# Kernel tuning notes

Hardware: AMD Instinct MI355X
Metric: run time of the kernel (lower is better)

The kernel has to match this reference:

```python
import jax, jax.numpy as jnp
import numpy as np
from jax import lax

B, T = 256, 64
X_DIMS, CCG_DIMS, H, N_TAG = 512, 256, 1024, 512
DIN = X_DIMS + CCG_DIMS
PAD = 0


def setup_inputs() -> dict:
    key = jax.random.key(0)
    ks = jax.random.split(key, 12)
    emb = jax.random.normal(ks[0], (N_TAG, CCG_DIMS), jnp.float32)
    emb = emb.at[PAD].set(0.0)  # padding_idx row is zero
    s_ih = 1.0 / np.sqrt(H)
    return {
        "x": jax.random.normal(ks[1], (B, X_DIMS), jnp.float32),
        "atom_truth": jax.random.randint(ks[2], (B, T), 0, N_TAG),
        "atom_mask": jax.random.randint(ks[3], (B, T), 0, 2).astype(bool),
        "emb": emb,
        "W_ih": jax.random.normal(ks[4], (4 * H, DIN), jnp.float32) * s_ih,
        "W_hh": jax.random.normal(ks[5], (4 * H, H), jnp.float32) * s_ih,
        "b_ih": jax.random.normal(ks[6], (4 * H,), jnp.float32) * s_ih,
        "b_hh": jax.random.normal(ks[7], (4 * H,), jnp.float32) * s_ih,
        "W_out": jax.random.normal(ks[8], (N_TAG, H), jnp.float32) * s_ih,
        "b_out": jax.random.normal(ks[9], (N_TAG,), jnp.float32) * s_ih,
        "h0": jax.random.normal(ks[10], (B, H), jnp.float32),
        "c0": jax.random.normal(ks[11], (B, H), jnp.float32),
    }


def reference(x, atom_truth, atom_mask, emb, W_ih, W_hh, b_ih, b_hh, W_out, b_out, h0, c0):
    b, t = atom_truth.shape
    # teacher forcing: step 0 uses token 0, step k uses atom_truth[:, k-1]
    prev_tok = jnp.concatenate([jnp.zeros((b, 1), atom_truth.dtype), atom_truth[:, :-1]], axis=1)
    ccg = emb[prev_tok]                                      # [B,T,E]
    inp = jnp.concatenate([jnp.broadcast_to(x[:, None, :], (b, t, x.shape[1])), ccg], axis=-1)
    # precompute input projection for all steps: [B,T,4H]
    xproj = jnp.einsum('btd,gd->btg', inp, W_ih) + b_ih + b_hh

    def cell(carry, xt):                                     # xt: [B,4H]
        h, c = carry
        gates = xt + h @ W_hh.T
        i, f, g, o = jnp.split(gates, 4, axis=-1)            # torch gate order i,f,g,o
        i, f, o = jax.nn.sigmoid(i), jax.nn.sigmoid(f), jax.nn.sigmoid(o)
        g = jnp.tanh(g)
        c = f * c + i * g
        h = o * jnp.tanh(c)
        return (h, c), h

    _, hs = lax.scan(cell, (h0, c0), jnp.swapaxes(xproj, 0, 1))  # hs: [T,B,H]
    logits = hs @ W_out.T + b_out                            # [T,B,N_TAG]
    logp = jax.nn.log_softmax(logits, axis=-1)
    tgt = atom_truth.T                                       # [T,B]
    nll = -jnp.take_along_axis(logp, tgt[..., None], axis=-1)[..., 0]  # [T,B]
    mask = atom_mask.T.astype(nll.dtype)
    return jnp.sum(nll * mask) / jnp.sum(mask)


if __name__ == "__main__":
    print(reference(**setup_inputs()))
```

## Files before the change

kernel.cpp:

```cpp
#include <hip/hip_runtime.h>
#include <hip/hip_bf16.h>

#define BB 256
#define TT 64
#define XD 512
#define CCG 256
#define DINk 768
#define HH 1024
#define G4 4096
#define NTAG 512

typedef float f32x4 __attribute__((ext_vector_type(4)));
typedef short s16x8 __attribute__((ext_vector_type(8)));
typedef short s16x4 __attribute__((ext_vector_type(4)));

#define WS_HS    0ull
#define WS_XBASE (WS_HS + (size_t)(TT+1)*BB*HH*2)
#define WS_EPROJ (WS_XBASE + (size_t)BB*G4*4)
#define WS_WIH   (WS_EPROJ + (size_t)NTAG*G4*4)
#define WS_WOUT  (WS_WIH + (size_t)G4*DINk*2)
#define WS_XBF   (WS_WOUT + (size_t)NTAG*HH*2)
#define WS_EMBBF (WS_XBF + (size_t)BB*XD*2)
#define WS_CNT   (WS_EMBBF + (size_t)NTAG*CCG*2)
#define WS_ACC   (WS_CNT + 1024)
#define WS_FLAG  (WS_ACC + 64)
#define WS_XPROJ (WS_FLAG + 64)

static __device__ __forceinline__ short f2bf(float f) {
  __hip_bfloat16 h = __float2bfloat16(f);
  return __builtin_bit_cast(short, h);
}
static __device__ __forceinline__ float bf2f(unsigned short u) {
  unsigned x = ((unsigned)u) << 16;
  return __builtin_bit_cast(float, x);
}
static __device__ __forceinline__ void store_dword_cc(void* p, unsigned v) {
  asm volatile("global_store_dword %0, %1, off sc0 sc1" :: "v"(p), "v"(v) : "memory");
}
static __device__ __forceinline__ void store_short_cc(void* p, unsigned v) {
  asm volatile("global_store_short %0, %1, off sc0 sc1" :: "v"(p), "v"(v) : "memory");
}
static __device__ __forceinline__ int load_int_cc(const void* p) {
  int r;
  asm volatile("global_load_dword %0, %1, off sc0 sc1\n\ts_waitcnt vmcnt(0)"
               : "=v"(r) : "v"(p) : "memory");
  return r;
}
static __device__ __forceinline__ float fsig(float x) {
  return __builtin_amdgcn_rcpf(1.f + __expf(-x));
}
static __device__ __forceinline__ float ftanh(float x) {
  return 1.f - 2.f * __builtin_amdgcn_rcpf(1.f + __expf(2.f * x));
}

__global__ void k_f2bf8(const float* __restrict__ in, short* __restrict__ out, int n8) {
  int i = blockIdx.x * blockDim.x + threadIdx.x;
  if (i >= n8) return;
  size_t idx = (size_t)i * 8;
  float4 a = *(const float4*)(in + idx);
  float4 b = *(const float4*)(in + idx + 4);
  s16x8 o;
  o[0]=f2bf(a.x); o[1]=f2bf(a.y); o[2]=f2bf(a.z); o[3]=f2bf(a.w);
  o[4]=f2bf(b.x); o[5]=f2bf(b.y); o[6]=f2bf(b.z); o[7]=f2bf(b.w);
  *(s16x8*)(out + idx) = o;
}

__global__ void k_init(const float* __restrict__ h0, const int* __restrict__ mask_as_int,
                       char* __restrict__ ws) {
  int tid = blockIdx.x * blockDim.x + threadIdx.x;
  short* hb0 = (short*)(ws + WS_HS);
  for (int i = tid; i < BB * HH; i += gridDim.x * blockDim.x) hb0[i] = f2bf(h0[i]);
  if (blockIdx.x == 0) {
    int* cnt = (int*)(ws + WS_CNT);
    for (int i = threadIdx.x; i < 256; i += blockDim.x) cnt[i] = 0;
    int v = 0;
    for (int i = threadIdx.x; i < 4096; i += blockDim.x) v |= (mask_as_int[i] & ~1);
    __shared__ int red[256];
    red[threadIdx.x] = v;
    __syncthreads();
    if (threadIdx.x == 0) {
      int a = 0;
      for (int j = 0; j < 256; j++) a |= red[j];
      ((int*)(ws + WS_FLAG))[0] = (a != 0) ? 1 : 0;
      float* acc = (float*)(ws + WS_ACC);
      acc[0] = 0.f; acc[1] = 0.f;
    }
  }
}

__global__ __launch_bounds__(256) void k_gemm(const short* __restrict__ A, int lda,
    const short* __restrict__ Bm, int ldb, int bcol0,
    short* __restrict__ C, int ldc, int ksteps,
    const float* __restrict__ bias1, const float* __restrict__ bias2) {
  int w = threadIdx.x >> 6, l = threadIdx.x & 63;
  int lc = l & 15, lq = l >> 4;
  int arow = blockIdx.x * 64 + w * 16 + lc;
  f32x4 acc[4];
  const f32x4 z = {0.f, 0.f, 0.f, 0.f};
#pragma unroll
  for (int i = 0; i < 4; i++) acc[i] = z;
  const short* ap = A + (size_t)arow * lda + lq * 8;
  for (int kk = 0; kk < ksteps; ++kk) {
    s16x8 a = *(const s16x8*)(ap + kk * 32);
#pragma unroll
    for (int nt = 0; nt < 4; ++nt) {
      int brow = blockIdx.y * 64 + nt * 16 + lc;
      s16x8 b = *(const s16x8*)(Bm + (size_t)brow * ldb + bcol0 + kk * 32 + lq * 8);
      acc[nt] = __builtin_amdgcn_mfma_f32_16x16x32_bf16(a, b, acc[nt], 0, 0, 0);
    }
  }
#pragma unroll
  for (int nt = 0; nt < 4; ++nt) {
    int col = blockIdx.y * 64 + nt * 16 + lc;
    float badd = (bias1 ? bias1[col] : 0.f) + (bias2 ? bias2[col] : 0.f);
#pragma unroll
    for (int j = 0; j < 4; j++) {
      int r = blockIdx.x * 64 + w * 16 + lq * 4 + j;
      C[(size_t)r * ldc + col] = f2bf(acc[nt][j] + badd);
    }
  }
}

__global__ __launch_bounds__(256) void k_xproj_t(const short* __restrict__ xb,
    const short* __restrict__ ep, const int* __restrict__ atruth,
    short* __restrict__ out) {
  __shared__ short tile[64 * 264];
  const int cc = blockIdx.x, g = blockIdx.y, t = blockIdx.z;
  const int b = threadIdx.x;
  const int tok = (t == 0) ? 0 : atruth[b * TT + t - 1];
  const int gc0 = g * 1024 + cc * 64;
  const short* xs = xb + (size_t)b * G4 + gc0;
  const short* es = ep + (size_t)tok * G4 + gc0;
#pragma unroll
  for (int i = 0; i < 64; i += 8) {
    s16x8 xv = *(const s16x8*)(xs + i);
    s16x8 ev = *(const s16x8*)(es + i);
#pragma unroll
    for (int j = 0; j < 8; ++j)
      tile[(i + j) * 264 + b] = f2bf(bf2f((unsigned short)xv[j]) + bf2f((unsigned short)ev[j]));
  }
  __syncthreads();
  const int c = threadIdx.x >> 2, b0 = (threadIdx.x & 3) * 64;
  short* dst = out + ((size_t)t * G4 + gc0 + c) * BB + b0;
  const short* src = tile + c * 264 + b0;
#pragma unroll
  for (int i = 0; i < 64; i += 8) *(s16x8*)(dst + i) = *(const s16x8*)(src + i);
}

__global__ __launch_bounds__(512, 2) void k_lstm(const float* __restrict__ Whh,
    const short* __restrict__ xproj, const float* __restrict__ c0,
    char* __restrict__ ws) {
  extern __shared__ char sm[];
  float* part = (float*)(sm + 131072);
  const int bid = blockIdx.x;
  const int xcd = bid & 7, slot = bid >> 3;
  const int mg = xcd >> 1;
  const int hb = slot * 2 + (xcd & 1);
  const int wgid = (xcd & 1) * 32 + slot;
  const int tid = threadIdx.x;
  const int w = tid >> 6, l = tid & 63;
  const int lc = l & 15, lq = l >> 4;
  const int wy = w & 3, kh = w >> 2;

  {
    const int r = tid >> 3, q = tid & 7;
    const int g = r >> 4, rl = r & 15;
    const float* src = Whh + (size_t)(g * HH + hb * 16 + rl) * HH + q * 128;
    const int swz = (rl & 7) << 4;
    char* dst = sm + r * 2048;
#pragma unroll
    for (int i = 0; i < 128; i += 8) {
      float4 f0 = *(const float4*)(src + i);
      float4 f1 = *(const float4*)(src + i + 4);
      s16x8 o;
      o[0]=f2bf(f0.x); o[1]=f2bf(f0.y); o[2]=f2bf(f0.z); o[3]=f2bf(f0.w);
      o[4]=f2bf(f1.x); o[5]=f2bf(f1.y); o[6]=f2bf(f1.z); o[7]=f2bf(f1.w);
      int koff = (q * 128 + i) * 2;
      *(s16x8*)(dst + (koff ^ swz)) = o;
    }
  }

  const int colbase = hb * 16;
  short* hs = (short*)(ws + WS_HS);
  int* flags = (int*)(ws + WS_CNT);
  const int swzl = (lc & 7) << 4;
  const int row0 = mg * 64 + wy * 16;

  float cst[4];
  s16x4 xg0, xg1, xg2, xg3, xn0, xn1, xn2, xn3;
  if (kh == 0) {
#pragma unroll
    for (int j = 0; j < 4; ++j)
      cst[j] = c0[(size_t)(row0 + lq * 4 + j) * HH + colbase + lc];
    const short* xp = xproj + ((size_t)colbase + lc) * BB + row0 + lq * 4;
    xg0 = *(const s16x4*)(xp);
    xg1 = *(const s16x4*)(xp + (size_t)1024 * BB);
    xg2 = *(const s16x4*)(xp + (size_t)2048 * BB);
    xg3 = *(const s16x4*)(xp + (size_t)3072 * BB);
  }
  float* pslot = part + (size_t)wy * 1024 + l;
  __syncthreads();

  for (int t = 0; t < TT; ++t) {
    if (t && w == 0) {
      const int* f = flags + mg * 64 + l;
      for (;;) {
        int v = load_int_cc(f);
        if (__all(v >= t)) break;
        __builtin_amdgcn_s_sleep(1);
      }
    }
    __syncthreads();

    if (kh == 0 && t + 1 < TT) {
      const short* xp = xproj + ((size_t)(t + 1) * G4 + colbase + lc) * BB + row0 + lq * 4;
      xn0 = *(const s16x4*)(xp);
      xn1 = *(const s16x4*)(xp + (size_t)1024 * BB);
      xn2 = *(const s16x4*)(xp + (size_t)2048 * BB);
      xn3 = *(const s16x4*)(xp + (size_t)3072 * BB);
    }

    const short* arowp = hs + (size_t)t * (BB * HH) + (size_t)(row0 + lc) * HH + kh * 512 + lq * 8;
    s16x8 areg[16];
#pragma unroll
    for (int kk = 0; kk < 16; ++kk) areg[kk] = *(const s16x8*)(arowp + kk * 32);

    const f32x4 z = {0.f, 0.f, 0.f, 0.f};
    f32x4 acc0 = z, acc1 = z, acc2 = z, acc3 = z;
#pragma unroll
    for (int kk = 0; kk < 16; ++kk) {
      const int kx = (((kh * 16 + kk) * 64) + lq * 16) ^ swzl;
      const char* bp = sm + lc * 2048 + kx;
      acc0 = __builtin_amdgcn_mfma_f32_16x16x32_bf16(areg[kk], *(const s16x8*)(bp), acc0, 0, 0, 0);
      acc1 = __builtin_amdgcn_mfma_f32_16x16x32_bf16(areg[kk], *(const s16x8*)(bp + 16 * 2048), acc1, 0, 0, 0);
      acc2 = __builtin_amdgcn_mfma_f32_16x16x32_bf16(areg[kk], *(const s16x8*)(bp + 32 * 2048), acc2, 0, 0, 0);
      acc3 = __builtin_amdgcn_mfma_f32_16x16x32_bf16(areg[kk], *(const s16x8*)(bp + 48 * 2048), acc3, 0, 0, 0);
    }

    if (kh == 1) {
#pragma unroll
      for (int j = 0; j < 4; ++j) {
        pslot[(0 * 4 + j) * 64] = acc0[j];
        pslot[(1 * 4 + j) * 64] = acc1[j];
        pslot[(2 * 4 + j) * 64] = acc2[j];
        pslot[(3 * 4 + j) * 64] = acc3[j];
      }
    }
    __syncthreads();

    if (kh == 0) {
#pragma unroll
      for (int j = 0; j < 4; ++j) {
        acc0[j] += pslot[(0 * 4 + j) * 64];
        acc1[j] += pslot[(1 * 4 + j) * 64];
        acc2[j] += pslot[(2 * 4 + j) * 64];
        acc3[j] += pslot[(3 * 4 + j) * 64];
      }
      short* hrow = hs + (size_t)(t + 1) * (BB * HH) +
                    (size_t)(row0 + lq * 4) * HH + colbase + lc;
#pragma unroll
      for (int j = 0; j < 4; ++j) {
        float pi = acc0[j] + bf2f((unsigned short)xg0[j]);
        float pf = acc1[j] + bf2f((unsigned short)xg1[j]);
        float pg = acc2[j] + bf2f((unsigned short)xg2[j]);
        float po = acc3[j] + bf2f((unsigned short)xg3[j]);
        float cv = fsig(pf) * cst[j] + fsig(pi) * ftanh(pg);
        cst[j] = cv;
        store_short_cc(hrow + (size_t)j * HH, (unsigned)(unsigned short)f2bf(fsig(po) * ftanh(cv)));
      }
      xg0 = xn0; xg1 = xn1; xg2 = xn2; xg3 = xn3;
    }
    asm volatile("s_waitcnt vmcnt(0)" ::: "memory");
    __syncthreads();
    if (tid == 0 && t < TT - 1) store_dword_cc(flags + mg * 64 + wgid, t + 1);
  }
}

__global__ __launch_bounds__(256, 1) void k_logits(const short* __restrict__ hsb,
    const short* __restrict__ Wo, const float* __restrict__ bout,
    const int* __restrict__ atruth, const void* __restrict__ maskp,
    char* __restrict__ ws) {
  extern __shared__ char sm[];
  const int tid = threadIdx.x;
  const int w = tid >> 6, l = tid & 63;
  const int lc = l & 15, lq = l >> 4;
  const int rowbase = blockIdx.x * 64 + w * 16;
  f32x4 acc[32];
#pragma unroll
  for (int nt = 0; nt < 32; ++nt) {
    float bv = bout[nt * 16 + lc];
    f32x4 tmp = {bv, bv, bv, bv};
    acc[nt] = tmp;
  }
  const int swzl = (lc & 7) << 4;
  for (int kb = 0; kb < 16; ++kb) {
    __syncthreads();
    {
      const int r0 = tid >> 3, q = tid & 7;
#pragma unroll
      for (int i = 0; i < 16; i++) {
        int r = r0 + 32 * i;
        s16x8 v = *(const s16x8*)(Wo + (size_t)r * HH + kb * 64 + q * 8);
        *(s16x8*)(sm + r * 128 + ((q * 16) ^ ((r & 7) << 4))) = v;
      }
    }
    __syncthreads();
#pragma unroll
    for (int ks = 0; ks < 2; ++ks) {
      s16x8 a = *(const s16x8*)(hsb + (size_t)(rowbase + lc) * HH + kb * 64 + ks * 32 + lq * 8);
      const int kx = (ks * 64 + lq * 16) ^ swzl;
#pragma unroll
      for (int nt = 0; nt < 32; ++nt) {
        s16x8 b = *(const s16x8*)(sm + (nt * 16 + lc) * 128 + kx);
        acc[nt] = __builtin_amdgcn_mfma_f32_16x16x32_bf16(a, b, acc[nt], 0, 0, 0);
      }
    }
  }
  const int bytemode = ((const int*)(ws + WS_FLAG))[0];
  const unsigned char* mb = (const unsigned char*)maskp;
  const int* mi = (const int*)maskp;
  float nlls = 0.f, cnts = 0.f;
#pragma unroll
  for (int j = 0; j < 4; j++) {
    int gr = rowbase + lq * 4 + j;
    int tt = gr >> 8, b = gr & 255;
    float m = -1e30f;
#pragma unroll
    for (int nt = 0; nt < 32; ++nt) m = fmaxf(m, acc[nt][j]);
    m = fmaxf(m, __shfl_xor(m, 1)); m = fmaxf(m, __shfl_xor(m, 2));
    m = fmaxf(m, __shfl_xor(m, 4)); m = fmaxf(m, __shfl_xor(m, 8));
    float s = 0.f;
#pragma unroll
    for (int nt = 0; nt < 32; ++nt) s += __expf(acc[nt][j] - m);
    s += __shfl_xor(s, 1); s += __shfl_xor(s, 2);
    s += __shfl_xor(s, 4); s += __shfl_xor(s, 8);
    float lse = m + __logf(s);
    int tg = atruth[b * TT + tt];
    int mk = bytemode ? (int)mb[b * TT + tt] : mi[b * TT + tt];
    if (((tg & 15) == lc) && mk) {
      float tl = 0.f;
#pragma unroll
      for (int nt = 0; nt < 32; ++nt) if (nt == (tg >> 4)) tl = acc[nt][j];
      nlls += (lse - tl);
    }
    if (lc == 0 && mk) cnts += 1.f;
  }
#pragma unroll
  for (int off = 1; off < 64; off <<= 1) {
    nlls += __shfl_xor(nlls, off);
    cnts += __shfl_xor(cnts, off);
  }
  if (l == 0) {
    float* accf = (float*)(ws + WS_ACC);
    atomicAdd(&accf[0], nlls);
    atomicAdd(&accf[1], cnts);
  }
}

__global__ void k_final(const char* __restrict__ ws, float* __restrict__ out) {
  const float* accf = (const float*)(ws + WS_ACC);
  out[0] = accf[0] / accf[1];
}

extern "C" void kernel_launch(void* const* d_in, const int* in_sizes, int n_in,
                              void* d_out, int out_size, void* d_ws, size_t ws_size,
                              hipStream_t stream) {
  const float* x      = (const float*)d_in[0];
  const int*   atruth = (const int*)d_in[1];
  const void*  amask  = d_in[2];
  const float* emb    = (const float*)d_in[3];
  const float* W_ih   = (const float*)d_in[4];
  const float* W_hh   = (const float*)d_in[5];
  const float* b_ih   = (const float*)d_in[6];
  const float* b_hh   = (const float*)d_in[7];
  const float* W_out  = (const float*)d_in[8];
  const float* b_out  = (const float*)d_in[9];
  const float* h0     = (const float*)d_in[10];
  const float* c0     = (const float*)d_in[11];
  char* ws = (char*)d_ws;
  float* out = (float*)d_out;

  hipFuncSetAttribute((const void*)k_lstm, hipFuncAttributeMaxDynamicSharedMemorySize, 147456);
  hipFuncSetAttribute((const void*)k_logits, hipFuncAttributeMaxDynamicSharedMemorySize, 65536);

  k_f2bf8<<<dim3((G4 * DINk / 8 + 255) / 256), 256, 0, stream>>>(W_ih, (short*)(ws + WS_WIH), G4 * DINk / 8);
  k_f2bf8<<<dim3((NTAG * HH / 8 + 255) / 256), 256, 0, stream>>>(W_out, (short*)(ws + WS_WOUT), NTAG * HH / 8);
  k_f2bf8<<<dim3((BB * XD / 8 + 255) / 256), 256, 0, stream>>>(x, (short*)(ws + WS_XBF), BB * XD / 8);
  k_f2bf8<<<dim3((NTAG * CCG / 8 + 255) / 256), 256, 0, stream>>>(emb, (short*)(ws + WS_EMBBF), NTAG * CCG / 8);

  k_init<<<64, 256, 0, stream>>>(h0, (const int*)amask, ws);

  k_gemm<<<dim3(4, 64), 256, 0, stream>>>((short*)(ws + WS_XBF), XD, (short*)(ws + WS_WIH), DINk, 0,
                                          (short*)(ws + WS_XBASE), G4, XD / 32, b_ih, b_hh);
  k_gemm<<<dim3(8, 64), 256, 0, stream>>>((short*)(ws + WS_EMBBF), CCG, (short*)(ws + WS_WIH), DINk, XD,
                                          (short*)(ws + WS_EPROJ), G4, CCG / 32, nullptr, nullptr);

  k_xproj_t<<<dim3(16, 4, 64), 256, 0, stream>>>((const short*)(ws + WS_XBASE),
                                                 (const short*)(ws + WS_EPROJ), atruth,
                                                 (short*)(ws + WS_XPROJ));

  k_lstm<<<256, 512, 147456, stream>>>(W_hh, (const short*)(ws + WS_XPROJ), c0, ws);

  k_logits<<<256, 256, 65536, stream>>>((short*)(ws + WS_HS) + BB * HH, (short*)(ws + WS_WOUT), b_out,
                                        atruth, amask, ws);
  k_final<<<1, 1, 0, stream>>>(ws, out);
}
```

Before: 629.8 us.

## Fuse embedding-projection gather into LSTM kernel, drop xproj transpose kernel

Removes the separate kernel that built a transposed per-timestep input projection and instead gathers the token's precomputed embedding projection inside the recurrent kernel. The idle second K-half warps prefetch the next step's embedding rows into a shared-memory buffer while the first half holds the time-invariant x-projection in registers. The A-operand loads are also moved back into the MFMA loop instead of being preloaded into 16 registers. This removes a large intermediate write and read, but adds per-step gathers and LDS traffic on the serial critical path, and raises shared memory per block.

```diff
diff --git a/kernel.cpp b/kernel.cpp
--- a/kernel.cpp
+++ b/kernel.cpp
@@ -12,7 +12,6 @@
 
 typedef float f32x4 __attribute__((ext_vector_type(4)));
 typedef short s16x8 __attribute__((ext_vector_type(8)));
-typedef short s16x4 __attribute__((ext_vector_type(4)));
 
 #define WS_HS    0ull
 #define WS_XBASE (WS_HS + (size_t)(TT+1)*BB*HH*2)
@@ -24,7 +23,6 @@
 #define WS_CNT   (WS_EMBBF + (size_t)NTAG*CCG*2)
 #define WS_ACC   (WS_CNT + 1024)
 #define WS_FLAG  (WS_ACC + 64)
-#define WS_XPROJ (WS_FLAG + 64)
 
 static __device__ __forceinline__ short f2bf(float f) {
   __hip_bfloat16 h = __float2bfloat16(f);
@@ -121,37 +119,13 @@
   }
 }
 
-__global__ __launch_bounds__(256) void k_xproj_t(const short* __restrict__ xb,
-    const short* __restrict__ ep, const int* __restrict__ atruth,
-    short* __restrict__ out) {
-  __shared__ short tile[64 * 264];
-  const int cc = blockIdx.x, g = blockIdx.y, t = blockIdx.z;
-  const int b = threadIdx.x;
-  const int tok = (t == 0) ? 0 : atruth[b * TT + t - 1];
-  const int gc0 = g * 1024 + cc * 64;
-  const short* xs = xb + (size_t)b * G4 + gc0;
-  const short* es = ep + (size_t)tok * G4 + gc0;
-#pragma unroll
-  for (int i = 0; i < 64; i += 8) {
-    s16x8 xv = *(const s16x8*)(xs + i);
-    s16x8 ev = *(const s16x8*)(es + i);
-#pragma unroll
-    for (int j = 0; j < 8; ++j)
-      tile[(i + j) * 264 + b] = f2bf(bf2f((unsigned short)xv[j]) + bf2f((unsigned short)ev[j]));
-  }
-  __syncthreads();
-  const int c = threadIdx.x >> 2, b0 = (threadIdx.x & 3) * 64;
-  short* dst = out + ((size_t)t * G4 + gc0 + c) * BB + b0;
-  const short* src = tile + c * 264 + b0;
-#pragma unroll
-  for (int i = 0; i < 64; i += 8) *(s16x8*)(dst + i) = *(const s16x8*)(src + i);
-}
-
-__global__ __launch_bounds__(512, 2) void k_lstm(const float* __restrict__ Whh,
-    const short* __restrict__ xproj, const float* __restrict__ c0,
+__global__ __launch_bounds__(512) void k_lstm(const float* __restrict__ Whh,
+    const short* __restrict__ xbase, const short* __restrict__ eproj,
+    const int* __restrict__ atruth, const float* __restrict__ c0,
     char* __restrict__ ws) {
   extern __shared__ char sm[];
   float* part = (float*)(sm + 131072);
+  short* xbuf = (short*)(sm + 131072 + 16384);
   const int bid = blockIdx.x;
   const int xcd = bid & 7, slot = bid >> 3;
   const int mg = xcd >> 1;
@@ -186,17 +160,24 @@
   const int swzl = (lc & 7) << 4;
   const int row0 = mg * 64 + wy * 16;
 
-  float cst[4];
-  s16x4 xg0, xg1, xg2, xg3, xn0, xn1, xn2, xn3;
+  float cst[4], xbv[4][4];
   if (kh == 0) {
 #pragma unroll
-    for (int j = 0; j < 4; ++j)
-      cst[j] = c0[(size_t)(row0 + lq * 4 + j) * HH + colbase + lc];
-    const short* xp = xproj + ((size_t)colbase + lc) * BB + row0 + lq * 4;
-    xg0 = *(const s16x4*)(xp);
-    xg1 = *(const s16x4*)(xp + (size_t)1024 * BB);
-    xg2 = *(const s16x4*)(xp + (size_t)2048 * BB);
-    xg3 = *(const s16x4*)(xp + (size_t)3072 * BB);
+    for (int j = 0; j < 4; ++j) {
+      const int b = row0 + lq * 4 + j;
+      cst[j] = c0[(size_t)b * HH + colbase + lc];
+#pragma unroll
+      for (int g = 0; g < 4; ++g)
+        xbv[g][j] = bf2f((unsigned short)xbase[(size_t)b * G4 + g * HH + colbase + lc]);
+    }
+  }
+  if (kh == 1) {
+    const int tid2 = tid - 256, grow = tid2 >> 2, ggate = tid2 & 3;
+    const short* es = eproj + (size_t)ggate * HH + colbase;
+    s16x8 e0 = *(const s16x8*)(es);
+    s16x8 e1 = *(const s16x8*)(es + 8);
+    *(s16x8*)(xbuf + grow * 66 + ggate * 16) = e0;
+    *(s16x8*)(xbuf + grow * 66 + ggate * 16 + 8) = e1;
   }
   float* pslot = part + (size_t)wy * 1024 + l;
   __syncthreads();
@@ -212,29 +193,35 @@
     }
     __syncthreads();
 
-    if (kh == 0 && t + 1 < TT) {
-      const short* xp = xproj + ((size_t)(t + 1) * G4 + colbase + lc) * BB + row0 + lq * 4;
-      xn0 = *(const s16x4*)(xp);
-      xn1 = *(const s16x4*)(xp + (size_t)1024 * BB);
-      xn2 = *(const s16x4*)(xp + (size_t)2048 * BB);
-      xn3 = *(const s16x4*)(xp + (size_t)3072 * BB);
-    }
-
-    const short* arowp = hs + (size_t)t * (BB * HH) + (size_t)(row0 + lc) * HH + kh * 512 + lq * 8;
-    s16x8 areg[16];
-#pragma unroll
-    for (int kk = 0; kk < 16; ++kk) areg[kk] = *(const s16x8*)(arowp + kk * 32);
+    s16x8 e0, e1;
+    if (kh == 1 && t + 1 < TT) {
+      const int tid2 = tid - 256, grow = tid2 >> 2, ggate = tid2 & 3;
+      int tokn = atruth[(mg * 64 + grow) * TT + t];
+      const short* es = eproj + (size_t)tokn * G4 + ggate * HH + colbase;
+      e0 = *(const s16x8*)(es);
+      e1 = *(const s16x8*)(es + 8);
+    }
+    float exv[4][4];
+    if (kh == 0) {
+#pragma unroll
+      for (int g = 0; g < 4; ++g)
+#pragma unroll
+        for (int j = 0; j < 4; ++j)
+          exv[g][j] = bf2f((unsigned short)xbuf[(wy * 16 + lq * 4 + j) * 66 + g * 16 + lc]);
+    }
 
     const f32x4 z = {0.f, 0.f, 0.f, 0.f};
     f32x4 acc0 = z, acc1 = z, acc2 = z, acc3 = z;
+    const short* arowp = hs + (size_t)t * (BB * HH) + (size_t)(row0 + lc) * HH + kh * 512 + lq * 8;
 #pragma unroll
     for (int kk = 0; kk < 16; ++kk) {
+      s16x8 a = *(const s16x8*)(arowp + kk * 32);
       const int kx = (((kh * 16 + kk) * 64) + lq * 16) ^ swzl;
       const char* bp = sm + lc * 2048 + kx;
-      acc0 = __builtin_amdgcn_mfma_f32_16x16x32_bf16(areg[kk], *(const s16x8*)(bp), acc0, 0, 0, 0);
-      acc1 = __builtin_amdgcn_mfma_f32_16x16x32_bf16(areg[kk], *(const s16x8*)(bp + 16 * 2048), acc1, 0, 0, 0);
-      acc2 = __builtin_amdgcn_mfma_f32_16x16x32_bf16(areg[kk], *(const s16x8*)(bp + 32 * 2048), acc2, 0, 0, 0);
-      acc3 = __builtin_amdgcn_mfma_f32_16x16x32_bf16(areg[kk], *(const s16x8*)(bp + 48 * 2048), acc3, 0, 0, 0);
+      acc0 = __builtin_amdgcn_mfma_f32_16x16x32_bf16(a, *(const s16x8*)(bp), acc0, 0, 0, 0);
+      acc1 = __builtin_amdgcn_mfma_f32_16x16x32_bf16(a, *(const s16x8*)(bp + 16 * 2048), acc1, 0, 0, 0);
+      acc2 = __builtin_amdgcn_mfma_f32_16x16x32_bf16(a, *(const s16x8*)(bp + 32 * 2048), acc2, 0, 0, 0);
+      acc3 = __builtin_amdgcn_mfma_f32_16x16x32_bf16(a, *(const s16x8*)(bp + 48 * 2048), acc3, 0, 0, 0);
     }
 
     if (kh == 1) {
@@ -260,15 +247,18 @@
                     (size_t)(row0 + lq * 4) * HH + colbase + lc;
 #pragma unroll
       for (int j = 0; j < 4; ++j) {
-        float pi = acc0[j] + bf2f((unsigned short)xg0[j]);
-        float pf = acc1[j] + bf2f((unsigned short)xg1[j]);
-        float pg = acc2[j] + bf2f((unsigned short)xg2[j]);
-        float po = acc3[j] + bf2f((unsigned short)xg3[j]);
+        float pi = acc0[j] + exv[0][j] + xbv[0][j];
+        float pf = acc1[j] + exv[1][j] + xbv[1][j];
+        float pg = acc2[j] + exv[2][j] + xbv[2][j];
+        float po = acc3[j] + exv[3][j] + xbv[3][j];
         float cv = fsig(pf) * cst[j] + fsig(pi) * ftanh(pg);
         cst[j] = cv;
         store_short_cc(hrow + (size_t)j * HH, (unsigned)(unsigned short)f2bf(fsig(po) * ftanh(cv)));
       }
-      xg0 = xn0; xg1 = xn1; xg2 = xn2; xg3 = xn3;
+    } else if (t + 1 < TT) {
+      const int tid2 = tid - 256, grow = tid2 >> 2, ggate = tid2 & 3;
+      *(s16x8*)(xbuf + grow * 66 + ggate * 16) = e0;
+      *(s16x8*)(xbuf + grow * 66 + ggate * 16 + 8) = e1;
     }
     asm volatile("s_waitcnt vmcnt(0)" ::: "memory");
     __syncthreads();
@@ -380,7 +370,7 @@
   char* ws = (char*)d_ws;
   float* out = (float*)d_out;
 
-  hipFuncSetAttribute((const void*)k_lstm, hipFuncAttributeMaxDynamicSharedMemorySize, 147456);
+  hipFuncSetAttribute((const void*)k_lstm, hipFuncAttributeMaxDynamicSharedMemorySize, 155904);
   hipFuncSetAttribute((const void*)k_logits, hipFuncAttributeMaxDynamicSharedMemorySize, 65536);
 
   k_f2bf8<<<dim3((G4 * DINk / 8 + 255) / 256), 256, 0, stream>>>(W_ih, (short*)(ws + WS_WIH), G4 * DINk / 8);
@@ -395,11 +385,8 @@
   k_gemm<<<dim3(8, 64), 256, 0, stream>>>((short*)(ws + WS_EMBBF), CCG, (short*)(ws + WS_WIH), DINk, XD,
                                           (short*)(ws + WS_EPROJ), G4, CCG / 32, nullptr, nullptr);
 
-  k_xproj_t<<<dim3(16, 4, 64), 256, 0, stream>>>((const short*)(ws + WS_XBASE),
-                                                 (const short*)(ws + WS_EPROJ), atruth,
-                                                 (short*)(ws + WS_XPROJ));
-
-  k_lstm<<<256, 512, 147456, stream>>>(W_hh, (const short*)(ws + WS_XPROJ), c0, ws);
+  k_lstm<<<256, 512, 155904, stream>>>(W_hh, (const short*)(ws + WS_XBASE),
+                                       (const short*)(ws + WS_EPROJ), atruth, c0, ws);
 
   k_logits<<<256, 256, 65536, stream>>>((short*)(ws + WS_HS) + BB * HH, (short*)(ws + WS_WOUT), b_out,
                                         atruth, amask, ws);
```

Result: faster. 549.4 us, median of 3 (-12.8%).
